# Performance work log

Hardware: AMD Instinct MI355X
Metric: run time of the kernel (lower is better)

The kernel has to match this reference:

```python
import jax, jax.numpy as jnp
import numpy as np

B, S, D_MODEL, N_HEADS = 4, 2048, 1024, 16
HEAD_DIM = D_MODEL // N_HEADS  # 64; used only for the softmax scale, as in the source


def setup_inputs() -> dict:
    key = jax.random.key(0)
    kq, kk, kv, kw = jax.random.split(key, 4)
    q = jax.random.normal(kq, (B, S, D_MODEL), dtype=jnp.float32)
    k = jax.random.normal(kk, (B, S, D_MODEL), dtype=jnp.float32)
    v = jax.random.normal(kv, (B, S, D_MODEL), dtype=jnp.float32)
    # out_proj: nn.Linear(d_model, d_model, bias=False) -> weight [out, in]
    W_out = jax.random.normal(kw, (D_MODEL, D_MODEL), dtype=jnp.float32) * (1.0 / np.sqrt(D_MODEL))
    return {"q": q, "k": k, "v": v, "W_out": W_out}


def reference(q, k, v, W_out):
    scale = 1.0 / jnp.sqrt(jnp.float32(HEAD_DIM))
    # scores: [B, Sq, Sk] -- full quadratic score matrix, as in the source
    scores = jnp.einsum("bqd,bkd->bqk", q, k) * scale
    attn = jax.nn.softmax(scores, axis=-1)
    out = jnp.einsum("bqk,bkd->bqd", attn, v)
    # torch Linear: y = x @ W^T
    return jnp.einsum("bsd,ed->bse", out, W_out)
```

## Files before the change

kernel.cpp:

```cpp
#include <hip/hip_runtime.h>
#include <hip/hip_fp16.h>
#include <stdint.h>

typedef _Float16 h16;
typedef _Float16 h16x8 __attribute__((ext_vector_type(8)));
typedef float f32x4 __attribute__((ext_vector_type(4)));

#define BB 4
#define SS 2048
#define DD 1024

#define EPI_H16 0
#define EPI_EXP 1
#define EPI_DIV 2

__device__ __forceinline__ void gload16(const void* g, void* l) {
    __builtin_amdgcn_global_load_lds(
        (const __attribute__((address_space(1))) uint32_t*)g,
        (__attribute__((address_space(3))) uint32_t*)l, 16, 0, 0);
}

__global__ __launch_bounds__(256) void cvt_all(
    const float* __restrict__ q, const float* __restrict__ k,
    const float* __restrict__ v, const float* __restrict__ w,
    h16* __restrict__ qh, h16* __restrict__ kh,
    h16* __restrict__ vh, h16* __restrict__ wh) {
    int b = blockIdx.x;
    const float* src; h16* dst; float sc = 1.0f;
    if (b < 2048)      { src = q; dst = qh; sc = 0.125f; }
    else if (b < 4096) { src = k; dst = kh; b -= 2048; }
    else if (b < 6144) { src = v; dst = vh; b -= 4096; }
    else               { src = w; dst = wh; b -= 6144; }
    size_t base = (size_t)b * 1024 + threadIdx.x;
#pragma unroll
    for (int i = 0; i < 4; ++i) {
        size_t g = base + (size_t)i * 256;
        float4 a = ((const float4*)src)[g];
        union { int2 i2; h16 h[4]; } u;
        u.h[0] = (h16)(a.x * sc); u.h[1] = (h16)(a.y * sc);
        u.h[2] = (h16)(a.z * sc); u.h[3] = (h16)(a.w * sc);
        ((int2*)dst)[g] = u.i2;
    }
}

template<int BM, int EPI>
__global__ __launch_bounds__(512, 2) void gemm2p(
    const h16* __restrict__ A, const h16* __restrict__ B, void* __restrict__ Cv,
    int lda, int ldb, int ldc, int K, int tilesN, int tilesMN,
    long long aBatch, long long bBatch, long long cBatch, const float* __restrict__ rsum)
{
    constexpr int WROWS  = BM / 2;
    constexpr int MF     = WROWS / 16;
    constexpr int MH     = MF / 2;
    constexpr int AH     = WROWS / 2;
    constexpr int AL     = BM / 128;
    constexpr int ABYTES = BM * 128;
    constexpr int BBYTES = 256 * 128;
    constexpr int BUFB   = ABYTES + BBYTES;

    __shared__ __align__(1024) char lds[2 * BUFB];

    const int tid = threadIdx.x;
    const int nwg = gridDim.x;
    const int bid = blockIdx.x;
    const int wgid = (bid & 7) * (nwg >> 3) + (bid >> 3);
    const int bb  = wgid / tilesMN;
    const int rem = wgid % tilesMN;
    const int tm = rem / tilesN, tn = rem % tilesN;
    const int row0 = tm * BM, col0 = tn * 256;

    const h16* Ab = A + (long long)bb * aBatch;
    const h16* Bb = B + (long long)bb * bBatch;

    const int lane = tid & 63, wid = tid >> 6;
    const int wm = wid >> 2, wn = wid & 3;
    const int frow = lane & 15, kq = lane >> 4;

    const int NT = K >> 6;

    f32x4 acc[MF][4];
#pragma unroll
    for (int m = 0; m < MF; ++m)
#pragma unroll
        for (int n = 0; n < 4; ++n) acc[m][n] = (f32x4){0.f, 0.f, 0.f, 0.f};

    char* l0 = (char*)lds;

    auto STAGE_B = [&](int kt, int buf) {
#pragma unroll
        for (int i = 0; i < 4; ++i) {
            int d = i * 512 + tid;
            int s = d & 7, r = d >> 3;
            int gg = s ^ (r & 7);
            gload16(Bb + (size_t)(col0 + r) * ldb + kt + gg * 8,
                    l0 + buf * BUFB + ABYTES + (r * 8 + s) * 16);
        }
    };
    auto STAGE_AH = [&](int kt, int buf, int mh) {
#pragma unroll
        for (int i = 0; i < AL; ++i) {
            int d = i * 512 + tid;
            int s = d & 7, hr = d >> 3;
            int r = ((hr & ~(AH - 1)) << 1) + mh * AH + (hr & (AH - 1));
            int gg = s ^ (r & 7);
            gload16(Ab + (size_t)(row0 + r) * lda + kt + gg * 8,
                    l0 + buf * BUFB + (r * 8 + s) * 16);
        }
    };
    auto READ_A = [&](int buf, int mh, h16x8 (&af)[MH][2]) {
#pragma unroll
        for (int mm = 0; mm < MH; ++mm)
#pragma unroll
            for (int ks = 0; ks < 2; ++ks) {
                int r = wm * WROWS + (mh * MH + mm) * 16 + frow;
                int s = (ks * 4 + kq) ^ (r & 7);
                af[mm][ks] = *(const h16x8*)(l0 + buf * BUFB + (r * 8 + s) * 16);
            }
    };
    auto READ_B = [&](int buf, h16x8 (&bf)[4][2]) {
#pragma unroll
        for (int nn = 0; nn < 4; ++nn)
#pragma unroll
            for (int ks = 0; ks < 2; ++ks) {
                int r = wn * 64 + nn * 16 + frow;
                int s = (ks * 4 + kq) ^ (r & 7);
                bf[nn][ks] = *(const h16x8*)(l0 + buf * BUFB + ABYTES + (r * 8 + s) * 16);
            }
    };
    auto MFMA_H = [&](int mh, h16x8 (&af)[MH][2], h16x8 (&bf)[4][2]) {
        __builtin_amdgcn_s_setprio(1);
#pragma unroll
        for (int ks = 0; ks < 2; ++ks)
#pragma unroll
            for (int mm = 0; mm < MH; ++mm)
#pragma unroll
                for (int nn = 0; nn < 4; ++nn)
                    acc[mh * MH + mm][nn] =
                        __builtin_amdgcn_mfma_f32_16x16x32_f16(
                            af[mm][ks], bf[nn][ks], acc[mh * MH + mm][nn], 0, 0, 0);
        __builtin_amdgcn_s_setprio(0);
    };

    STAGE_B(0, 0); STAGE_AH(0, 0, 0); STAGE_AH(0, 0, 1);
    if constexpr (BM == 256) asm volatile("s_waitcnt vmcnt(2)" ::: "memory");
    else                     asm volatile("s_waitcnt vmcnt(1)" ::: "memory");
    __builtin_amdgcn_s_barrier();

    h16x8 af[MH][2], bf[4][2];

    for (int G = 0; G < NT; ++G) {
        const int buf = G & 1;
        const int kt1 = (G + 1) << 6;
        if (G + 1 < NT) {
            STAGE_B(kt1, buf ^ 1);
            STAGE_AH(kt1, buf ^ 1, 0);
            STAGE_AH(kt1, buf ^ 1, 1);
        }
        READ_A(buf, 0, af);
        READ_B(buf, bf);
        MFMA_H(0, af, bf);
        if (G + 1 < NT) {
            if constexpr (BM == 256) asm volatile("s_waitcnt vmcnt(8)" ::: "memory");
            else                     asm volatile("s_waitcnt vmcnt(6)" ::: "memory");
        } else {
            asm volatile("s_waitcnt vmcnt(0)" ::: "memory");
        }
        __builtin_amdgcn_s_barrier();
        READ_A(buf, 1, af);
        MFMA_H(1, af, bf);
        if (G + 1 >= NT) break;
        if constexpr (BM == 256) asm volatile("s_waitcnt vmcnt(2)" ::: "memory");
        else                     asm volatile("s_waitcnt vmcnt(1)" ::: "memory");
        __builtin_amdgcn_s_barrier();
    }

    const int erow = row0 + wm * WROWS + (lane >> 4) * 4;
    const int ecol = col0 + wn * 64 + (lane & 15);
#pragma unroll
    for (int m = 0; m < MF; ++m)
#pragma unroll
        for (int n = 0; n < 4; ++n)
#pragma unroll
            for (int j = 0; j < 4; ++j) {
                int row = erow + m * 16 + j, col = ecol + n * 16;
                float vv = acc[m][n][j];
                if constexpr (EPI == EPI_EXP) {
                    h16* C = (h16*)Cv + (long long)bb * cBatch;
                    C[(size_t)row * ldc + col] = (h16)__expf(vv - 16.0f);
                } else if constexpr (EPI == EPI_DIV) {
                    float* C = (float*)Cv + (long long)bb * cBatch;
                    C[(size_t)row * ldc + col] = vv * rsum[bb * SS + row];
                } else {
                    h16* C = (h16*)Cv + (long long)bb * cBatch;
                    C[(size_t)row * ldc + col] = (h16)vv;
                }
            }
}

template<int EPI>
__global__ __launch_bounds__(256, 2) void gemm2p_sm(
    const h16* __restrict__ A, const h16* __restrict__ B, void* __restrict__ Cv,
    int lda, int ldb, int ldc, int K, int tilesN, int tilesMN,
    long long aBatch, long long bBatch, long long cBatch, const float* __restrict__ rsum)
{
    constexpr int ABYTES = 128 * 128;
    constexpr int BBYTES = 128 * 128;
    constexpr int BUFB   = ABYTES + BBYTES;

    __shared__ __align__(1024) char lds[2 * BUFB];

    const int tid = threadIdx.x;
    const int nwg = gridDim.x;
    const int bid = blockIdx.x;
    const int wgid = (bid & 7) * (nwg >> 3) + (bid >> 3);
    const int bb  = wgid / tilesMN;
    const int rem = wgid % tilesMN;
    const int tm = rem / tilesN, tn = rem % tilesN;
    const int row0 = tm * 128, col0 = tn * 128;

    const h16* Ab = A + (long long)bb * aBatch;
    const h16* Bb = B + (long long)bb * bBatch;

    const int lane = tid & 63, wid = tid >> 6;
    const int wm = wid >> 1, wn = wid & 1;
    const int frow = lane & 15, kq = lane >> 4;

    const int NT = K >> 6;

    f32x4 acc[4][4];
#pragma unroll
    for (int m = 0; m < 4; ++m)
#pragma unroll
        for (int n = 0; n < 4; ++n) acc[m][n] = (f32x4){0.f, 0.f, 0.f, 0.f};

    char* l0 = (char*)lds;

    auto STAGE_B = [&](int kt, int buf) {
#pragma unroll
        for (int i = 0; i < 4; ++i) {
            int d = i * 256 + tid;
            int s = d & 7, r = d >> 3;
            int gg = s ^ (r & 7);
            gload16(Bb + (size_t)(col0 + r) * ldb + kt + gg * 8,
                    l0 + buf * BUFB + ABYTES + (r * 8 + s) * 16);
        }
    };
    auto STAGE_AH = [&](int kt, int buf, int mh) {
#pragma unroll
        for (int i = 0; i < 2; ++i) {
            int d = i * 256 + tid;
            int s = d & 7, hr = d >> 3;
            int r = ((hr & ~31) << 1) + mh * 32 + (hr & 31);
            int gg = s ^ (r & 7);
            gload16(Ab + (size_t)(row0 + r) * lda + kt + gg * 8,
                    l0 + buf * BUFB + (r * 8 + s) * 16);
        }
    };
    auto READ_A = [&](int buf, int mh, h16x8 (&af)[2][2]) {
#pragma unroll
        for (int mm = 0; mm < 2; ++mm)
#pragma unroll
            for (int ks = 0; ks < 2; ++ks) {
                int r = wm * 64 + (mh * 2 + mm) * 16 + frow;
                int s = (ks * 4 + kq) ^ (r & 7);
                af[mm][ks] = *(const h16x8*)(l0 + buf * BUFB + (r * 8 + s) * 16);
            }
    };
    auto READ_B = [&](int buf, h16x8 (&bf)[4][2]) {
#pragma unroll
        for (int nn = 0; nn < 4; ++nn)
#pragma unroll
            for (int ks = 0; ks < 2; ++ks) {
                int r = wn * 64 + nn * 16 + frow;
                int s = (ks * 4 + kq) ^ (r & 7);
                bf[nn][ks] = *(const h16x8*)(l0 + buf * BUFB + ABYTES + (r * 8 + s) * 16);
            }
    };
    auto MFMA_H = [&](int mh, h16x8 (&af)[2][2], h16x8 (&bf)[4][2]) {
        __builtin_amdgcn_s_setprio(1);
#pragma unroll
        for (int ks = 0; ks < 2; ++ks)
#pragma unroll
            for (int mm = 0; mm < 2; ++mm)
#pragma unroll
                for (int nn = 0; nn < 4; ++nn)
                    acc[mh * 2 + mm][nn] =
                        __builtin_amdgcn_mfma_f32_16x16x32_f16(
                            af[mm][ks], bf[nn][ks], acc[mh * 2 + mm][nn], 0, 0, 0);
        __builtin_amdgcn_s_setprio(0);
    };

    STAGE_B(0, 0); STAGE_AH(0, 0, 0); STAGE_AH(0, 0, 1);
    asm volatile("s_waitcnt vmcnt(2)" ::: "memory");
    __builtin_amdgcn_s_barrier();

    h16x8 af[2][2], bf[4][2];

    for (int G = 0; G < NT; ++G) {
        const int buf = G & 1;
        const int kt1 = (G + 1) << 6;
        if (G + 1 < NT) {
            STAGE_B(kt1, buf ^ 1);
            STAGE_AH(kt1, buf ^ 1, 0);
            STAGE_AH(kt1, buf ^ 1, 1);
        }
        READ_A(buf, 0, af);
        READ_B(buf, bf);
        MFMA_H(0, af, bf);
        if (G + 1 < NT) asm volatile("s_waitcnt vmcnt(8)" ::: "memory");
        else            asm volatile("s_waitcnt vmcnt(0)" ::: "memory");
        __builtin_amdgcn_s_barrier();
        READ_A(buf, 1, af);
        MFMA_H(1, af, bf);
        if (G + 1 >= NT) break;
        asm volatile("s_waitcnt vmcnt(2)" ::: "memory");
        __builtin_amdgcn_s_barrier();
    }

    const int erow = row0 + wm * 64 + (lane >> 4) * 4;
    const int ecol = col0 + wn * 64 + (lane & 15);
#pragma unroll
    for (int m = 0; m < 4; ++m)
#pragma unroll
        for (int n = 0; n < 4; ++n)
#pragma unroll
            for (int j = 0; j < 4; ++j) {
                int row = erow + m * 16 + j, col = ecol + n * 16;
                float vv = acc[m][n][j];
                if constexpr (EPI == EPI_DIV) {
                    float* C = (float*)Cv + (long long)bb * cBatch;
                    C[(size_t)row * ldc + col] = vv * rsum[bb * SS + row];
                } else if constexpr (EPI == EPI_EXP) {
                    h16* C = (h16*)Cv + (long long)bb * cBatch;
                    C[(size_t)row * ldc + col] = (h16)__expf(vv - 16.0f);
                } else {
                    h16* C = (h16*)Cv + (long long)bb * cBatch;
                    C[(size_t)row * ldc + col] = (h16)vv;
                }
            }
}

__global__ __launch_bounds__(256) void rowsumE(const h16* __restrict__ sc,
                                               float* __restrict__ rsum) {
    const int row = blockIdx.x;
    const h16* rp = sc + (size_t)row * 2048;
    union { int4 i4; h16 h[8]; } u;
    u.i4 = ((const int4*)rp)[threadIdx.x];
    float s = 0.f;
#pragma unroll
    for (int j = 0; j < 8; ++j) s += (float)u.h[j];
#pragma unroll
    for (int off = 32; off; off >>= 1) s += __shfl_xor(s, off);
    __shared__ float ws[4];
    const int lane = threadIdx.x & 63, wid = threadIdx.x >> 6;
    if (lane == 0) ws[wid] = s;
    __syncthreads();
    if (threadIdx.x == 0)
        rsum[row] = 1.0f / (ws[0] + ws[1] + ws[2] + ws[3]);
}

extern "C" void kernel_launch(void* const* d_in, const int* in_sizes, int n_in,
                              void* d_out, int out_size, void* d_ws, size_t ws_size,
                              hipStream_t stream) {
    (void)in_sizes; (void)n_in; (void)out_size; (void)ws_size;
    const float* q = (const float*)d_in[0];
    const float* k = (const float*)d_in[1];
    const float* v = (const float*)d_in[2];
    const float* w = (const float*)d_in[3];
    float* out = (float*)d_out;

    const size_t QKV = (size_t)BB * SS * DD;
    h16* qh = (h16*)d_ws;
    h16* kh = qh + QKV;
    h16* vh = kh + QKV;
    h16* wh = vh + QKV;
    h16* sc = wh + (size_t)DD * DD;
    float* rsum = (float*)(sc + (size_t)BB * SS * SS);

    cvt_all<<<6400, 256, 0, stream>>>(q, k, v, w, qh, kh, vh, wh);

    gemm2p<256, EPI_EXP><<<256, 512, 0, stream>>>(
        qh, kh, (void*)sc, DD, DD, SS, DD, 8, 64,
        (long long)SS * DD, (long long)SS * DD, (long long)SS * SS, nullptr);

    rowsumE<<<BB * SS, 256, 0, stream>>>(sc, rsum);

    h16* vpT = qh;
    gemm2p_sm<EPI_H16><<<512, 256, 0, stream>>>(
        wh, vh, (void*)vpT, DD, DD, BB * SS, DD, 64, 512,
        0LL, 0LL, 0LL, nullptr);

    gemm2p_sm<EPI_DIV><<<512, 256, 0, stream>>>(
        sc, vpT, (void*)out, SS, BB * SS, DD, SS, 8, 128,
        (long long)SS * SS, (long long)SS, (long long)SS * DD, rsum);
}
```

Baseline: 134.3 us.

## Load QK^T A-operand fragments directly from global into registers, bypassing LDS

The score GEMM kernel no longer stages the A (query) tile through LDS. Each wave now loads its own A fragments straight from global memory into registers, while B stays double-buffered in LDS. LDS use per block is halved, and one barrier per K-step is dropped. The cost is uncoalesced 16-byte global loads for A, extra vector registers to hold 16 fragments, and a full vmcnt(0) wait each iteration that may expose global latency.

```diff
diff --git a/kernel.cpp b/kernel.cpp
--- a/kernel.cpp
+++ b/kernel.cpp
@@ -43,22 +43,14 @@
     }
 }
 
-template<int BM, int EPI>
-__global__ __launch_bounds__(512, 2) void gemm2p(
+template<int EPI>
+__global__ __launch_bounds__(512, 2) void gemm_adz(
     const h16* __restrict__ A, const h16* __restrict__ B, void* __restrict__ Cv,
     int lda, int ldb, int ldc, int K, int tilesN, int tilesMN,
     long long aBatch, long long bBatch, long long cBatch, const float* __restrict__ rsum)
 {
-    constexpr int WROWS  = BM / 2;
-    constexpr int MF     = WROWS / 16;
-    constexpr int MH     = MF / 2;
-    constexpr int AH     = WROWS / 2;
-    constexpr int AL     = BM / 128;
-    constexpr int ABYTES = BM * 128;
-    constexpr int BBYTES = 256 * 128;
-    constexpr int BUFB   = ABYTES + BBYTES;
-
-    __shared__ __align__(1024) char lds[2 * BUFB];
+    constexpr int BBYT = 256 * 64 * 2;
+    __shared__ __align__(1024) char lds[2 * BBYT];
 
     const int tid = threadIdx.x;
     const int nwg = gridDim.x;
@@ -67,7 +59,7 @@
     const int bb  = wgid / tilesMN;
     const int rem = wgid % tilesMN;
     const int tm = rem / tilesN, tn = rem % tilesN;
-    const int row0 = tm * BM, col0 = tn * 256;
+    const int row0 = tm * 256, col0 = tn * 256;
 
     const h16* Ab = A + (long long)bb * aBatch;
     const h16* Bb = B + (long long)bb * bBatch;
@@ -78,9 +70,9 @@
 
     const int NT = K >> 6;
 
-    f32x4 acc[MF][4];
-#pragma unroll
-    for (int m = 0; m < MF; ++m)
+    f32x4 acc[8][4];
+#pragma unroll
+    for (int m = 0; m < 8; ++m)
 #pragma unroll
         for (int n = 0; n < 4; ++n) acc[m][n] = (f32x4){0.f, 0.f, 0.f, 0.f};
 
@@ -93,91 +85,68 @@
             int s = d & 7, r = d >> 3;
             int gg = s ^ (r & 7);
             gload16(Bb + (size_t)(col0 + r) * ldb + kt + gg * 8,
-                    l0 + buf * BUFB + ABYTES + (r * 8 + s) * 16);
-        }
-    };
-    auto STAGE_AH = [&](int kt, int buf, int mh) {
-#pragma unroll
-        for (int i = 0; i < AL; ++i) {
-            int d = i * 512 + tid;
-            int s = d & 7, hr = d >> 3;
-            int r = ((hr & ~(AH - 1)) << 1) + mh * AH + (hr & (AH - 1));
-            int gg = s ^ (r & 7);
-            gload16(Ab + (size_t)(row0 + r) * lda + kt + gg * 8,
-                    l0 + buf * BUFB + (r * 8 + s) * 16);
-        }
-    };
-    auto READ_A = [&](int buf, int mh, h16x8 (&af)[MH][2]) {
-#pragma unroll
-        for (int mm = 0; mm < MH; ++mm)
+                    l0 + buf * BBYT + (r * 8 + s) * 16);
+        }
+    };
+    h16x8 af[16];
+    auto LOAD_A_H = [&](int kt, int mh) {
+#pragma unroll
+        for (int mm = 0; mm < 4; ++mm)
 #pragma unroll
             for (int ks = 0; ks < 2; ++ks) {
-                int r = wm * WROWS + (mh * MH + mm) * 16 + frow;
-                int s = (ks * 4 + kq) ^ (r & 7);
-                af[mm][ks] = *(const h16x8*)(l0 + buf * BUFB + (r * 8 + s) * 16);
-            }
-    };
-    auto READ_B = [&](int buf, h16x8 (&bf)[4][2]) {
+                int r = row0 + wm * 128 + (mh * 4 + mm) * 16 + frow;
+                af[(mh * 4 + mm) * 2 + ks] =
+                    *(const h16x8*)(Ab + (size_t)r * lda + kt + (ks * 4 + kq) * 8);
+            }
+    };
+    h16x8 bf[4][2];
+    auto READ_B = [&](int buf) {
 #pragma unroll
         for (int nn = 0; nn < 4; ++nn)
 #pragma unroll
             for (int ks = 0; ks < 2; ++ks) {
                 int r = wn * 64 + nn * 16 + frow;
                 int s = (ks * 4 + kq) ^ (r & 7);
-                bf[nn][ks] = *(const h16x8*)(l0 + buf * BUFB + ABYTES + (r * 8 + s) * 16);
-            }
-    };
-    auto MFMA_H = [&](int mh, h16x8 (&af)[MH][2], h16x8 (&bf)[4][2]) {
+                bf[nn][ks] = *(const h16x8*)(l0 + buf * BBYT + (r * 8 + s) * 16);
+            }
+    };
+    auto MFMA_H = [&](int mh) {
         __builtin_amdgcn_s_setprio(1);
 #pragma unroll
-        for (int ks = 0; ks < 2; ++ks)
-#pragma unroll
-            for (int mm = 0; mm < MH; ++mm)
-#pragma unroll
-                for (int nn = 0; nn < 4; ++nn)
-                    acc[mh * MH + mm][nn] =
-                        __builtin_amdgcn_mfma_f32_16x16x32_f16(
-                            af[mm][ks], bf[nn][ks], acc[mh * MH + mm][nn], 0, 0, 0);
+        for (int mm = 0; mm < 4; ++mm)
+#pragma unroll
+            for (int nn = 0; nn < 4; ++nn)
+#pragma unroll
+                for (int ks = 0; ks < 2; ++ks)
+                    acc[mh * 4 + mm][nn] = __builtin_amdgcn_mfma_f32_16x16x32_f16(
+                        af[(mh * 4 + mm) * 2 + ks], bf[nn][ks], acc[mh * 4 + mm][nn], 0, 0, 0);
         __builtin_amdgcn_s_setprio(0);
     };
 
-    STAGE_B(0, 0); STAGE_AH(0, 0, 0); STAGE_AH(0, 0, 1);
-    if constexpr (BM == 256) asm volatile("s_waitcnt vmcnt(2)" ::: "memory");
-    else                     asm volatile("s_waitcnt vmcnt(1)" ::: "memory");
+    STAGE_B(0, 0);
+    LOAD_A_H(0, 0); LOAD_A_H(0, 1);
+    asm volatile("s_waitcnt vmcnt(0)" ::: "memory");
     __builtin_amdgcn_s_barrier();
-
-    h16x8 af[MH][2], bf[4][2];
 
     for (int G = 0; G < NT; ++G) {
         const int buf = G & 1;
         const int kt1 = (G + 1) << 6;
+        if (G + 1 < NT) STAGE_B(kt1, buf ^ 1);
+        READ_B(buf);
+        MFMA_H(0);
+        if (G + 1 < NT) LOAD_A_H(kt1, 0);
+        MFMA_H(1);
         if (G + 1 < NT) {
-            STAGE_B(kt1, buf ^ 1);
-            STAGE_AH(kt1, buf ^ 1, 0);
-            STAGE_AH(kt1, buf ^ 1, 1);
-        }
-        READ_A(buf, 0, af);
-        READ_B(buf, bf);
-        MFMA_H(0, af, bf);
-        if (G + 1 < NT) {
-            if constexpr (BM == 256) asm volatile("s_waitcnt vmcnt(8)" ::: "memory");
-            else                     asm volatile("s_waitcnt vmcnt(6)" ::: "memory");
-        } else {
+            LOAD_A_H(kt1, 1);
             asm volatile("s_waitcnt vmcnt(0)" ::: "memory");
-        }
-        __builtin_amdgcn_s_barrier();
-        READ_A(buf, 1, af);
-        MFMA_H(1, af, bf);
-        if (G + 1 >= NT) break;
-        if constexpr (BM == 256) asm volatile("s_waitcnt vmcnt(2)" ::: "memory");
-        else                     asm volatile("s_waitcnt vmcnt(1)" ::: "memory");
-        __builtin_amdgcn_s_barrier();
+            __builtin_amdgcn_s_barrier();
+        }
     }
 
-    const int erow = row0 + wm * WROWS + (lane >> 4) * 4;
+    const int erow = row0 + wm * 128 + (lane >> 4) * 4;
     const int ecol = col0 + wn * 64 + (lane & 15);
 #pragma unroll
-    for (int m = 0; m < MF; ++m)
+    for (int m = 0; m < 8; ++m)
 #pragma unroll
         for (int n = 0; n < 4; ++n)
 #pragma unroll
@@ -379,7 +348,7 @@
 
     cvt_all<<<6400, 256, 0, stream>>>(q, k, v, w, qh, kh, vh, wh);
 
-    gemm2p<256, EPI_EXP><<<256, 512, 0, stream>>>(
+    gemm_adz<EPI_EXP><<<256, 512, 0, stream>>>(
         qh, kh, (void*)sc, DD, DD, SS, DD, 8, 64,
         (long long)SS * DD, (long long)SS * DD, (long long)SS * SS, nullptr);
 
```

Measured after the change: 180.0 us. +34.0%, slower.
